# Optimization experiments

Hardware: AMD Instinct MI355X
Metric: run time of the kernel (lower is better)

The kernel has to match this reference:

```python
import jax, jax.numpy as jnp
import numpy as np

N = 100000          # active voxels
KS = 7              # kernel size per spatial dim
K = KS ** 3         # 343 kernel offsets
G = 64              # voxel grid extent
INPLANES = 128
PLANES = 128
D2 = PLANES // 4    # 32
EPS = 1e-5


def _build_neighbor_map(seed=0):
    # Random distinct voxel coordinates in a G^3 grid, then for every point and
    # every 7^3 offset find the index of the neighboring voxel (-1 if absent).
    rng = np.random.default_rng(seed)
    lin = rng.choice(G ** 3, size=N, replace=False)
    coords = np.stack(np.unravel_index(lin, (G, G, G)), axis=1).astype(np.int64)  # [N,3]
    keys = coords[:, 0] * G * G + coords[:, 1] * G + coords[:, 2]
    order = np.argsort(keys)
    skeys = keys[order]
    offs = np.arange(KS) - KS // 2
    off_grid = np.stack(np.meshgrid(offs, offs, offs, indexing='ij'), axis=-1).reshape(K, 3)
    q = coords[:, None, :] + off_grid[None, :, :]          # [N,K,3]
    inb = np.all((q >= 0) & (q < G), axis=-1)
    qk = q[..., 0] * G * G + q[..., 1] * G + q[..., 2]
    pos = np.searchsorted(skeys, qk)
    pos_c = np.clip(pos, 0, N - 1)
    found = inb & (skeys[pos_c] == qk)
    nbr = np.where(found, order[pos_c], -1).astype(np.int32)  # [N,K]
    return jnp.asarray(nbr)


def setup_inputs() -> dict:
    key = jax.random.key(0)
    k = jax.random.split(key, 4)
    feats = jax.random.normal(k[0], (N, INPLANES), jnp.float32)
    w1 = jax.random.normal(k[1], (INPLANES, D2), jnp.float32) / np.sqrt(INPLANES)
    w_conv = jax.random.normal(k[2], (K, D2, D2), jnp.float32) / np.sqrt(K * D2)
    w2 = jax.random.normal(k[3], (D2, PLANES), jnp.float32) / np.sqrt(D2)
    return {
        'feats': feats,
        'nbr': _build_neighbor_map(),
        'w1': w1,
        'ln1_g': jnp.ones((D2,), jnp.float32),
        'ln1_b': jnp.zeros((D2,), jnp.float32),
        'w_conv': w_conv,
        'w2': w2,
        'ln2_g': jnp.ones((PLANES,), jnp.float32),
        'ln2_b': jnp.zeros((PLANES,), jnp.float32),
    }


def _layernorm(x, g, b):
    m = jnp.mean(x, axis=-1, keepdims=True)
    v = jnp.var(x, axis=-1, keepdims=True)
    return (x - m) * jax.lax.rsqrt(v + EPS) * g + b


def _sparse_conv(x, nbr, w):
    # x: [N,d2], nbr: [N,K], w: [K,d2,d2]; gather-apply-scatter per kernel offset.
    def step(acc, inp):
        idx, wk = inp                                # idx: [N], wk: [d2,d2]
        valid = (idx >= 0).astype(x.dtype)[:, None]
        g = jnp.take(x, jnp.maximum(idx, 0), axis=0) * valid
        return acc + g @ wk, None
    acc0 = jnp.zeros((x.shape[0], w.shape[2]), x.dtype)
    out, _ = jax.lax.scan(step, acc0, (nbr.T, w))
    return out


def reference(feats, nbr, w1, ln1_g, ln1_b, w_conv, w2, ln2_g, ln2_b):
    shortcut = feats                                  # inplanes == planes -> Identity
    h = _layernorm(feats @ w1, ln1_g, ln1_b)          # unary_1: [N,d2]
    h = _sparse_conv(h, nbr, w_conv)                  # 7^3 sparse conv: [N,d2]
    h = _layernorm(h @ w2, ln2_g, ln2_b)              # unary_2: [N,planes]
    h = jax.nn.gelu(h, approximate=False)             # drop_path is Identity (rate 0)
    return h + shortcut
```

## Files before the change

kernel.cpp:

```cpp
#include <hip/hip_runtime.h>
#include <hip/hip_bf16.h>

#define N_PTS 100000
#define KOFF 343
#define EPS 1e-5f

typedef __hip_bfloat16 bf16;
typedef __attribute__((ext_vector_type(4))) float f32x4;
typedef __attribute__((ext_vector_type(16))) float f32x16;
typedef __attribute__((ext_vector_type(8))) short s16x8;

__global__ __launch_bounds__(256) void pack_kernel(const float* __restrict__ w_conv,
                                                   bf16* __restrict__ wpk) {
  int t = blockIdx.x * 256 + threadIdx.x;
  if (t >= KOFF * 128) return;
  int l = t & 63;
  int s = (t >> 6) & 1;
  int k = t >> 7;
  int col = l & 31;
  int kq = l >> 5;
  const float* wk = w_conv + k * 1024;
  s16x8 v;
  for (int j = 0; j < 8; ++j) {
    bf16 h = __float2bfloat16(wk[(s * 16 + kq * 8 + j) * 32 + col]);
    short sv;
    __builtin_memcpy(&sv, &h, 2);
    v[j] = sv;
  }
  *reinterpret_cast<s16x8*>(reinterpret_cast<char*>(wpk) + (size_t)t * 16) = v;
}

__global__ __launch_bounds__(256) void unary1_kernel(const float* __restrict__ feats,
    const float* __restrict__ w1, const float* __restrict__ g1,
    const float* __restrict__ b1, bf16* __restrict__ h1b) {
  __shared__ float sf[8][128];
  __shared__ float sw[128 * 32];
  int tid = threadIdx.x;
  int rbase = blockIdx.x * 8;
  for (int i = tid; i < 1024; i += 256)
    reinterpret_cast<f32x4*>(sw)[i] = reinterpret_cast<const f32x4*>(w1)[i];
  {
    int i = tid;
    int r = rbase + (i >> 5);
    f32x4 v = reinterpret_cast<const f32x4*>(feats)[(size_t)r * 32 + (i & 31)];
    reinterpret_cast<f32x4*>(&sf[0][0])[i] = v;
  }
  __syncthreads();
  int half = tid >> 5;
  int c = tid & 31;
  int r = rbase + half;
  const float* frow = sf[half];
  float acc = 0.f;
  #pragma unroll 8
  for (int kk = 0; kk < 128; ++kk)
    acc += frow[kk] * sw[kk * 32 + c];
  float s = acc, s2 = acc * acc;
  #pragma unroll
  for (int m = 16; m >= 1; m >>= 1) {
    s  += __shfl_xor(s,  m, 64);
    s2 += __shfl_xor(s2, m, 64);
  }
  float mean = s * (1.f / 32.f);
  float var  = s2 * (1.f / 32.f) - mean * mean;
  float y = (acc - mean) * rsqrtf(var + EPS) * g1[c] + b1[c];
  h1b[(size_t)r * 32 + c] = __float2bfloat16(y);
}

__global__ __launch_bounds__(256) void conv_kernel(const bf16* __restrict__ h1b,
    const int* __restrict__ nbr, const bf16* __restrict__ wpk,
    float* __restrict__ h2) {
  __shared__ int snbr[32 * 345];
  int tid = threadIdx.x;
  int wave = tid >> 6;
  int l = tid & 63;
  int col = l & 31;
  int kq = l >> 5;
  int pbase = blockIdx.x * 32;
  {
    const int* g = nbr + (size_t)pbase * KOFF;
    for (int i = tid; i < 32 * KOFF; i += 256) {
      unsigned row = (unsigned)i / KOFF;
      unsigned kk = (unsigned)i - row * KOFF;
      snbr[row * 345 + kk] = g[i];
    }
  }
  __syncthreads();
  int k0 = (KOFF * wave) >> 2;
  int k1 = (KOFF * (wave + 1)) >> 2;
  f32x16 acc;
  #pragma unroll
  for (int i = 0; i < 16; ++i) acc[i] = 0.f;
  const s16x8* wb = reinterpret_cast<const s16x8*>(wpk);
  const s16x8 zv = {0, 0, 0, 0, 0, 0, 0, 0};
  const int* myrow = snbr + col * 345;
  for (int kb = k0; kb < k1; kb += 4) {
    int id[4];
    s16x8 A0[4], A1[4], B0[4], B1[4];
    #pragma unroll
    for (int j = 0; j < 4; ++j) {
      int k = kb + j;
      id[j] = (k < k1) ? myrow[k] : -1;
    }
    #pragma unroll
    for (int j = 0; j < 4; ++j) {
      int k = kb + j;
      int kc = (k < k1) ? k : (k1 - 1);
      const s16x8* r = reinterpret_cast<const s16x8*>(h1b + (size_t)(id[j] < 0 ? 0 : id[j]) * 32);
      A0[j] = r[kq];
      A1[j] = r[2 + kq];
      B0[j] = wb[(size_t)kc * 128 + l];
      B1[j] = wb[(size_t)kc * 128 + 64 + l];
    }
    #pragma unroll
    for (int j = 0; j < 4; ++j) {
      s16x8 a0 = id[j] < 0 ? zv : A0[j];
      s16x8 a1 = id[j] < 0 ? zv : A1[j];
      acc = __builtin_amdgcn_mfma_f32_32x32x16_bf16(a0, B0[j], acc, 0, 0, 0);
      acc = __builtin_amdgcn_mfma_f32_32x32x16_bf16(a1, B1[j], acc, 0, 0, 0);
    }
  }
  __syncthreads();
  float* red = reinterpret_cast<float*>(snbr);
  #pragma unroll
  for (int reg = 0; reg < 16; ++reg) {
    int rrow = (reg & 3) + 8 * (reg >> 2) + 4 * kq;
    red[wave * 1024 + rrow * 32 + col] = acc[reg];
  }
  __syncthreads();
  const f32x4* rv = reinterpret_cast<const f32x4*>(red);
  f32x4 s = rv[tid] + rv[256 + tid] + rv[512 + tid] + rv[768 + tid];
  reinterpret_cast<f32x4*>(h2 + (size_t)pbase * 32)[tid] = s;
}

__global__ __launch_bounds__(256) void unary2_kernel(const float* __restrict__ h2,
    const float* __restrict__ w2, const float* __restrict__ g2,
    const float* __restrict__ b2, const float* __restrict__ feats,
    float* __restrict__ out) {
  int tid = threadIdx.x;
  int wave = tid >> 6;
  int l = tid & 63;
  int r = blockIdx.x * 4 + wave;
  const float* hrow = h2 + (size_t)r * 32;
  float acc0 = 0.f, acc1 = 0.f;
  #pragma unroll
  for (int q = 0; q < 8; ++q) {
    f32x4 hv = reinterpret_cast<const f32x4*>(hrow)[q];
    #pragma unroll
    for (int j = 0; j < 4; ++j) {
      int kk = q * 4 + j;
      float h = hv[j];
      acc0 += h * w2[kk * 128 + l];
      acc1 += h * w2[kk * 128 + 64 + l];
    }
  }
  float s = acc0 + acc1, s2 = acc0 * acc0 + acc1 * acc1;
  #pragma unroll
  for (int m = 32; m >= 1; m >>= 1) {
    s  += __shfl_xor(s,  m, 64);
    s2 += __shfl_xor(s2, m, 64);
  }
  float mean = s * (1.f / 128.f);
  float var  = s2 * (1.f / 128.f) - mean * mean;
  float inv = rsqrtf(var + EPS);
  float y0 = (acc0 - mean) * inv * g2[l] + b2[l];
  float y1 = (acc1 - mean) * inv * g2[64 + l] + b2[64 + l];
  float ge0 = 0.5f * y0 * (1.f + erff(y0 * 0.70710678118f));
  float ge1 = 0.5f * y1 * (1.f + erff(y1 * 0.70710678118f));
  out[(size_t)r * 128 + l]      = ge0 + feats[(size_t)r * 128 + l];
  out[(size_t)r * 128 + 64 + l] = ge1 + feats[(size_t)r * 128 + 64 + l];
}

extern "C" void kernel_launch(void* const* d_in, const int* in_sizes, int n_in,
                              void* d_out, int out_size, void* d_ws, size_t ws_size,
                              hipStream_t stream) {
  const float* feats  = (const float*)d_in[0];
  const int*   nbr    = (const int*)d_in[1];
  const float* w1     = (const float*)d_in[2];
  const float* ln1_g  = (const float*)d_in[3];
  const float* ln1_b  = (const float*)d_in[4];
  const float* w_conv = (const float*)d_in[5];
  const float* w2     = (const float*)d_in[6];
  const float* ln2_g  = (const float*)d_in[7];
  const float* ln2_b  = (const float*)d_in[8];
  float* out = (float*)d_out;
  char* ws = (char*)d_ws;
  bf16*  h1b = (bf16*)ws;
  bf16*  wpk = (bf16*)(ws + 6400000);
  float* h2  = (float*)(ws + 7102464);

  hipLaunchKernelGGL(pack_kernel,   dim3((KOFF * 128 + 255) / 256), dim3(256), 0, stream, w_conv, wpk);
  hipLaunchKernelGGL(unary1_kernel, dim3(N_PTS / 8),                dim3(256), 0, stream, feats, w1, ln1_g, ln1_b, h1b);
  hipLaunchKernelGGL(conv_kernel,   dim3(N_PTS / 32),               dim3(256), 0, stream, h1b, nbr, wpk, h2);
  hipLaunchKernelGGL(unary2_kernel, dim3(N_PTS / 4),                dim3(256), 0, stream, h2, w2, ln2_g, ln2_b, feats, out);
}
```

Baseline: 328.5 us.

## Transpose neighbor map and give each wave a full 32-point tile

Adds a kernel that transposes the [N,K] neighbor map into [K,N] so each wave can read neighbor indices for 32 points per offset with coalesced loads. The new conv kernel assigns one 32-point tile per wave over all 343 offsets, prefetching the next group of indices. This removes the LDS staging, the cross-wave reduction and the block barriers. The cost is an extra pass that reads and writes the full 137 MB index array, and the path runs only when the workspace is large enough.

Result: slower. 473.5 us (+44.1%).

```diff
diff --git a/kernel.cpp b/kernel.cpp
--- a/kernel.cpp
+++ b/kernel.cpp
@@ -4,6 +4,7 @@
 #define N_PTS 100000
 #define KOFF 343
 #define EPS 1e-5f
+#define NTILES 3125
 
 typedef __hip_bfloat16 bf16;
 typedef __attribute__((ext_vector_type(4))) float f32x4;
@@ -64,6 +65,86 @@
   float var  = s2 * (1.f / 32.f) - mean * mean;
   float y = (acc - mean) * rsqrtf(var + EPS) * g1[c] + b1[c];
   h1b[(size_t)r * 32 + c] = __float2bfloat16(y);
+}
+
+__global__ __launch_bounds__(256) void transpose_kernel(const int* __restrict__ nbr,
+                                                        int* __restrict__ nbrT) {
+  __shared__ int t[32][33];
+  int tx = threadIdx.x & 31;
+  int ty0 = threadIdx.x >> 5;
+  int n0 = blockIdx.x * 32;
+  int k0 = blockIdx.y * 32;
+  #pragma unroll
+  for (int q = 0; q < 4; ++q) {
+    int ty = ty0 + 8 * q;
+    int k = k0 + tx;
+    if (k < KOFF) t[ty][tx] = nbr[(size_t)(n0 + ty) * KOFF + k];
+  }
+  __syncthreads();
+  #pragma unroll
+  for (int q = 0; q < 4; ++q) {
+    int ky = ty0 + 8 * q;
+    if (k0 + ky < KOFF)
+      nbrT[(size_t)(k0 + ky) * N_PTS + n0 + tx] = t[tx][ky];
+  }
+}
+
+__global__ __launch_bounds__(256) void conv_t_kernel(const bf16* __restrict__ h1b,
+    const int* __restrict__ nbrT, const bf16* __restrict__ wpk,
+    float* __restrict__ h2) {
+  int tid = threadIdx.x;
+  int wave = tid >> 6;
+  int l = tid & 63;
+  int col = l & 31;
+  int kq = l >> 5;
+  int tile = blockIdx.x * 4 + wave;
+  if (tile >= NTILES) return;
+  int pbase = tile * 32;
+  const int* nbase = nbrT + pbase + col;
+  f32x16 acc;
+  #pragma unroll
+  for (int i = 0; i < 16; ++i) acc[i] = 0.f;
+  const s16x8* wb = reinterpret_cast<const s16x8*>(wpk);
+  const s16x8 zv = {0, 0, 0, 0, 0, 0, 0, 0};
+  int idc[4];
+  #pragma unroll
+  for (int j = 0; j < 4; ++j) idc[j] = nbase[(size_t)j * N_PTS];
+  for (int kb = 0; kb < KOFF; kb += 4) {
+    int idn[4];
+    #pragma unroll
+    for (int j = 0; j < 4; ++j) {
+      int kn = kb + 4 + j;
+      idn[j] = (kn < KOFF) ? nbase[(size_t)kn * N_PTS] : -1;
+    }
+    s16x8 A0[4], A1[4], B0[4], B1[4];
+    #pragma unroll
+    for (int j = 0; j < 4; ++j) {
+      int k = kb + j;
+      int kc = (k < KOFF) ? k : (KOFF - 1);
+      int id = (k < KOFF) ? idc[j] : -1;
+      const s16x8* r = reinterpret_cast<const s16x8*>(h1b + (size_t)(id < 0 ? 0 : id) * 32);
+      A0[j] = r[kq];
+      A1[j] = r[2 + kq];
+      B0[j] = wb[(size_t)kc * 128 + l];
+      B1[j] = wb[(size_t)kc * 128 + 64 + l];
+    }
+    #pragma unroll
+    for (int j = 0; j < 4; ++j) {
+      int k = kb + j;
+      int id = (k < KOFF) ? idc[j] : -1;
+      s16x8 a0 = id < 0 ? zv : A0[j];
+      s16x8 a1 = id < 0 ? zv : A1[j];
+      acc = __builtin_amdgcn_mfma_f32_32x32x16_bf16(a0, B0[j], acc, 0, 0, 0);
+      acc = __builtin_amdgcn_mfma_f32_32x32x16_bf16(a1, B1[j], acc, 0, 0, 0);
+    }
+    #pragma unroll
+    for (int j = 0; j < 4; ++j) idc[j] = idn[j];
+  }
+  #pragma unroll
+  for (int reg = 0; reg < 16; ++reg) {
+    int rrow = (reg & 3) + 8 * (reg >> 2) + 4 * kq;
+    h2[(size_t)(pbase + rrow) * 32 + col] = acc[reg];
+  }
 }
 
 __global__ __launch_bounds__(256) void conv_kernel(const bf16* __restrict__ h1b,
@@ -187,9 +268,16 @@
   bf16*  h1b = (bf16*)ws;
   bf16*  wpk = (bf16*)(ws + 6400000);
   float* h2  = (float*)(ws + 7102464);
+  int*   nbrT = (int*)(ws + 19902464);
+  const size_t need = 19902464ULL + 137200000ULL;
 
   hipLaunchKernelGGL(pack_kernel,   dim3((KOFF * 128 + 255) / 256), dim3(256), 0, stream, w_conv, wpk);
   hipLaunchKernelGGL(unary1_kernel, dim3(N_PTS / 8),                dim3(256), 0, stream, feats, w1, ln1_g, ln1_b, h1b);
-  hipLaunchKernelGGL(conv_kernel,   dim3(N_PTS / 32),               dim3(256), 0, stream, h1b, nbr, wpk, h2);
-  hipLaunchKernelGGL(unary2_kernel, dim3(N_PTS / 4),                dim3(256), 0, stream, h2, w2, ln2_g, ln2_b, feats, out);
-}
+  if (ws_size >= need) {
+    hipLaunchKernelGGL(transpose_kernel, dim3(NTILES, (KOFF + 31) / 32), dim3(256), 0, stream, nbr, nbrT);
+    hipLaunchKernelGGL(conv_t_kernel,    dim3((NTILES + 3) / 4),         dim3(256), 0, stream, h1b, nbrT, wpk, h2);
+  } else {
+    hipLaunchKernelGGL(conv_kernel,      dim3(NTILES),                   dim3(256), 0, stream, h1b, nbr, wpk, h2);
+  }
+  hipLaunchKernelGGL(unary2_kernel, dim3(N_PTS / 4), dim3(256), 0, stream, h2, w2, ln2_g, ln2_b, feats, out);
+}
```

## Transpose neighbor map and restructure conv to stream k-major indices

Applied to the files above, without the earlier changes.

Adds a kernel that transposes the [N,343] neighbor map into k-major layout in workspace. A new conv kernel uses it: each wave reads coalesced neighbor indices directly from global memory with a software prefetch two steps ahead, instead of staging the whole map in shared memory. Each block now covers two 32-point tiles, and each tile's offsets are split across two waves. This adds a full extra read and write of about 137 MB for the transpose, and falls back to the old kernel if the workspace is too small.

Result: slower. 455.8 us (+38.8%).

```diff
diff --git a/kernel.cpp b/kernel.cpp
--- a/kernel.cpp
+++ b/kernel.cpp
@@ -4,6 +4,7 @@
 #define N_PTS 100000
 #define KOFF 343
 #define EPS 1e-5f
+#define NTILES 3125
 
 typedef __hip_bfloat16 bf16;
 typedef __attribute__((ext_vector_type(4))) float f32x4;
@@ -64,6 +65,90 @@
   float var  = s2 * (1.f / 32.f) - mean * mean;
   float y = (acc - mean) * rsqrtf(var + EPS) * g1[c] + b1[c];
   h1b[(size_t)r * 32 + c] = __float2bfloat16(y);
+}
+
+__global__ __launch_bounds__(256) void transpose_kernel(const int* __restrict__ nbr,
+                                                        int* __restrict__ nbrT) {
+  __shared__ int t[32][129];
+  int n0 = blockIdx.x * 128;
+  int k0 = blockIdx.y * 32;
+  int tx = threadIdx.x & 31;
+  int ty = threadIdx.x >> 5;
+  int kmax = KOFF - k0;
+  #pragma unroll
+  for (int q = 0; q < 16; ++q) {
+    int r = ty + 8 * q;
+    int n = n0 + r;
+    if (n < N_PTS && tx < kmax) t[tx][r] = nbr[(size_t)n * KOFF + k0 + tx];
+  }
+  __syncthreads();
+  int wx = threadIdx.x & 127;
+  int wy = threadIdx.x >> 7;
+  #pragma unroll
+  for (int q = 0; q < 16; ++q) {
+    int kk = wy + 2 * q;
+    int n = n0 + wx;
+    if (kk < kmax && n < N_PTS) nbrT[(size_t)(k0 + kk) * N_PTS + n] = t[kk][wx];
+  }
+}
+
+__global__ __launch_bounds__(256, 6) void conv_t2_kernel(const bf16* __restrict__ h1b,
+    const int* __restrict__ nbrT, const bf16* __restrict__ wpk,
+    float* __restrict__ h2) {
+  __shared__ float red[4 * 1024];
+  int tid = threadIdx.x;
+  int wave = tid >> 6;
+  int l = tid & 63;
+  int col = l & 31;
+  int kq = l >> 5;
+  int tile = wave & 1;
+  int half = wave >> 1;
+  int pbase = blockIdx.x * 64 + tile * 32;
+  bool live = pbase < N_PTS;
+  const int* nbase = nbrT + pbase + col;
+  int k0 = (KOFF * half) >> 1;
+  int k1 = (KOFF * (half + 1)) >> 1;
+  f32x16 acc;
+  #pragma unroll
+  for (int i = 0; i < 16; ++i) acc[i] = 0.f;
+  const s16x8* wb = reinterpret_cast<const s16x8*>(wpk);
+  const s16x8 zv = {0, 0, 0, 0, 0, 0, 0, 0};
+  int id0 = live ? nbase[(size_t)k0 * N_PTS] : -1;
+  int id1 = (live && k0 + 1 < k1) ? nbase[(size_t)(k0 + 1) * N_PTS] : -1;
+  int id2 = (live && k0 + 2 < k1) ? nbase[(size_t)(k0 + 2) * N_PTS] : -1;
+  int id3 = (live && k0 + 3 < k1) ? nbase[(size_t)(k0 + 3) * N_PTS] : -1;
+  for (int kb = k0; kb < k1; kb += 2) {
+    int kc1 = (kb + 1 < k1) ? kb + 1 : kb;
+    const s16x8* r0 = reinterpret_cast<const s16x8*>(h1b + (size_t)(id0 < 0 ? 0 : id0) * 32);
+    const s16x8* r1 = reinterpret_cast<const s16x8*>(h1b + (size_t)(id1 < 0 ? 0 : id1) * 32);
+    s16x8 A00 = r0[kq], A01 = r0[2 + kq];
+    s16x8 A10 = r1[kq], A11 = r1[2 + kq];
+    s16x8 B00 = wb[(size_t)kb * 128 + l];
+    s16x8 B01 = wb[(size_t)kb * 128 + 64 + l];
+    s16x8 B10 = wb[(size_t)kc1 * 128 + l];
+    s16x8 B11 = wb[(size_t)kc1 * 128 + 64 + l];
+    int id4 = (live && kb + 4 < k1) ? nbase[(size_t)(kb + 4) * N_PTS] : -1;
+    int id5 = (live && kb + 5 < k1) ? nbase[(size_t)(kb + 5) * N_PTS] : -1;
+    s16x8 a;
+    a = id0 < 0 ? zv : A00; acc = __builtin_amdgcn_mfma_f32_32x32x16_bf16(a, B00, acc, 0, 0, 0);
+    a = id0 < 0 ? zv : A01; acc = __builtin_amdgcn_mfma_f32_32x32x16_bf16(a, B01, acc, 0, 0, 0);
+    a = id1 < 0 ? zv : A10; acc = __builtin_amdgcn_mfma_f32_32x32x16_bf16(a, B10, acc, 0, 0, 0);
+    a = id1 < 0 ? zv : A11; acc = __builtin_amdgcn_mfma_f32_32x32x16_bf16(a, B11, acc, 0, 0, 0);
+    id0 = id2; id1 = id3; id2 = id4; id3 = id5;
+  }
+  #pragma unroll
+  for (int reg = 0; reg < 16; ++reg) {
+    int rrow = (reg & 3) + 8 * (reg >> 2) + 4 * kq;
+    red[wave * 1024 + rrow * 32 + col] = acc[reg];
+  }
+  __syncthreads();
+  const f32x4* rv = reinterpret_cast<const f32x4*>(red);
+  f32x4 sA = rv[tid] + rv[512 + tid];
+  f32x4 sB = rv[256 + tid] + rv[768 + tid];
+  f32x4* o = reinterpret_cast<f32x4*>(h2 + (size_t)blockIdx.x * 2048);
+  int p0 = blockIdx.x * 64;
+  if (p0 + 32 <= N_PTS) o[tid] = sA;
+  if (p0 + 64 <= N_PTS) o[256 + tid] = sB;
 }
 
 __global__ __launch_bounds__(256) void conv_kernel(const bf16* __restrict__ h1b,
@@ -187,9 +272,16 @@
   bf16*  h1b = (bf16*)ws;
   bf16*  wpk = (bf16*)(ws + 6400000);
   float* h2  = (float*)(ws + 7102464);
+  int*   nbrT = (int*)(ws + 19902464);
+  const size_t need = 19902464ULL + 137200000ULL;
 
   hipLaunchKernelGGL(pack_kernel,   dim3((KOFF * 128 + 255) / 256), dim3(256), 0, stream, w_conv, wpk);
   hipLaunchKernelGGL(unary1_kernel, dim3(N_PTS / 8),                dim3(256), 0, stream, feats, w1, ln1_g, ln1_b, h1b);
-  hipLaunchKernelGGL(conv_kernel,   dim3(N_PTS / 32),               dim3(256), 0, stream, h1b, nbr, wpk, h2);
-  hipLaunchKernelGGL(unary2_kernel, dim3(N_PTS / 4),                dim3(256), 0, stream, h2, w2, ln2_g, ln2_b, feats, out);
-}
+  if (ws_size >= need) {
+    hipLaunchKernelGGL(transpose_kernel, dim3((N_PTS + 127) / 128, (KOFF + 31) / 32), dim3(256), 0, stream, nbr, nbrT);
+    hipLaunchKernelGGL(conv_t2_kernel,   dim3((NTILES + 1) / 2),                      dim3(256), 0, stream, h1b, nbrT, wpk, h2);
+  } else {
+    hipLaunchKernelGGL(conv_kernel,      dim3(NTILES),                                dim3(256), 0, stream, h1b, nbr, wpk, h2);
+  }
+  hipLaunchKernelGGL(unary2_kernel, dim3(N_PTS / 4), dim3(256), 0, stream, h2, w2, ln2_g, ln2_b, feats, out);
+}
```

## Stage neighbor indices in four rounds with zero-row sentinel to shrink LDS

Applied to the files above, without the earlier changes.

The conv kernel now stages the neighbor map in four chunks of about 86 offsets into a 16KB shared buffer, down from the full 44KB one, which allows higher occupancy (launch bounds request 4 blocks). Missing neighbors are remapped to a zero row appended after h1b, so the per-element select on invalid gathers goes away. Index loads for the next group are prefetched before the MFMAs. The cost is extra barriers between rounds and less overlap of index staging with compute.

Result: slower. 386.1 us (+17.5%).

```diff
diff --git a/kernel.cpp b/kernel.cpp
--- a/kernel.cpp
+++ b/kernel.cpp
@@ -4,6 +4,8 @@
 #define N_PTS 100000
 #define KOFF 343
 #define EPS 1e-5f
+#define NTILES 3125
+#define SSTRIDE 87
 
 typedef __hip_bfloat16 bf16;
 typedef __attribute__((ext_vector_type(4))) float f32x4;
@@ -37,6 +39,8 @@
   __shared__ float sw[128 * 32];
   int tid = threadIdx.x;
   int rbase = blockIdx.x * 8;
+  if (blockIdx.x == 0 && tid < 16)
+    reinterpret_cast<int*>(h1b)[N_PTS * 16 + tid] = 0;
   for (int i = tid; i < 1024; i += 256)
     reinterpret_cast<f32x4*>(sw)[i] = reinterpret_cast<const f32x4*>(w1)[i];
   {
@@ -66,61 +70,92 @@
   h1b[(size_t)r * 32 + c] = __float2bfloat16(y);
 }
 
-__global__ __launch_bounds__(256) void conv_kernel(const bf16* __restrict__ h1b,
+template<int KCNT, int KBASE>
+__device__ __forceinline__ void stage_round(const int* __restrict__ g,
+                                            int* __restrict__ snbr, int wave, int l) {
+  #pragma unroll
+  for (int rr = 0; rr < 8; ++rr) {
+    int row = wave * 8 + rr;
+    const int* src = g + row * KOFF + KBASE;
+    if (l < KCNT) {
+      int v = src[l];
+      snbr[row * SSTRIDE + l] = v < 0 ? N_PTS : v;
+    }
+    if (64 + l < KCNT) {
+      int v = src[64 + l];
+      snbr[row * SSTRIDE + 64 + l] = v < 0 ? N_PTS : v;
+    }
+  }
+}
+
+template<int KCNT, int KBASE>
+__device__ __forceinline__ void process_round(const int* __restrict__ snbr,
+    const bf16* __restrict__ h1b, const s16x8* __restrict__ wb,
+    f32x16& acc, int wave, int l, int col, int kq) {
+  int k0 = (KCNT * wave) >> 2;
+  int k1 = (KCNT * (wave + 1)) >> 2;
+  const int* myrow = snbr + col * SSTRIDE;
+  int id[4];
+  #pragma unroll
+  for (int j = 0; j < 4; ++j) id[j] = (k0 + j < k1) ? myrow[k0 + j] : N_PTS;
+  for (int kb = k0; kb < k1; kb += 4) {
+    s16x8 A0[4], A1[4], B0[4], B1[4];
+    #pragma unroll
+    for (int j = 0; j < 4; ++j) {
+      const s16x8* r = reinterpret_cast<const s16x8*>(h1b + (size_t)id[j] * 32);
+      A0[j] = r[kq];
+      A1[j] = r[2 + kq];
+      int kc = (kb + j < k1) ? kb + j : k1 - 1;
+      B0[j] = wb[(size_t)(KBASE + kc) * 128 + l];
+      B1[j] = wb[(size_t)(KBASE + kc) * 128 + 64 + l];
+    }
+    int idn[4];
+    #pragma unroll
+    for (int j = 0; j < 4; ++j) idn[j] = (kb + 4 + j < k1) ? myrow[kb + 4 + j] : N_PTS;
+    #pragma unroll
+    for (int j = 0; j < 4; ++j) {
+      acc = __builtin_amdgcn_mfma_f32_32x32x16_bf16(A0[j], B0[j], acc, 0, 0, 0);
+      acc = __builtin_amdgcn_mfma_f32_32x32x16_bf16(A1[j], B1[j], acc, 0, 0, 0);
+    }
+    #pragma unroll
+    for (int j = 0; j < 4; ++j) id[j] = idn[j];
+  }
+}
+
+__global__ __launch_bounds__(256, 4) void conv_s2_kernel(const bf16* __restrict__ h1b,
     const int* __restrict__ nbr, const bf16* __restrict__ wpk,
     float* __restrict__ h2) {
-  __shared__ int snbr[32 * 345];
+  __shared__ int sbuf[4096];
   int tid = threadIdx.x;
   int wave = tid >> 6;
   int l = tid & 63;
   int col = l & 31;
   int kq = l >> 5;
   int pbase = blockIdx.x * 32;
-  {
-    const int* g = nbr + (size_t)pbase * KOFF;
-    for (int i = tid; i < 32 * KOFF; i += 256) {
-      unsigned row = (unsigned)i / KOFF;
-      unsigned kk = (unsigned)i - row * KOFF;
-      snbr[row * 345 + kk] = g[i];
-    }
-  }
-  __syncthreads();
-  int k0 = (KOFF * wave) >> 2;
-  int k1 = (KOFF * (wave + 1)) >> 2;
+  const int* g = nbr + (size_t)pbase * KOFF;
+  const s16x8* wb = reinterpret_cast<const s16x8*>(wpk);
   f32x16 acc;
   #pragma unroll
   for (int i = 0; i < 16; ++i) acc[i] = 0.f;
-  const s16x8* wb = reinterpret_cast<const s16x8*>(wpk);
-  const s16x8 zv = {0, 0, 0, 0, 0, 0, 0, 0};
-  const int* myrow = snbr + col * 345;
-  for (int kb = k0; kb < k1; kb += 4) {
-    int id[4];
-    s16x8 A0[4], A1[4], B0[4], B1[4];
-    #pragma unroll
-    for (int j = 0; j < 4; ++j) {
-      int k = kb + j;
-      id[j] = (k < k1) ? myrow[k] : -1;
-    }
-    #pragma unroll
-    for (int j = 0; j < 4; ++j) {
-      int k = kb + j;
-      int kc = (k < k1) ? k : (k1 - 1);
-      const s16x8* r = reinterpret_cast<const s16x8*>(h1b + (size_t)(id[j] < 0 ? 0 : id[j]) * 32);
-      A0[j] = r[kq];
-      A1[j] = r[2 + kq];
-      B0[j] = wb[(size_t)kc * 128 + l];
-      B1[j] = wb[(size_t)kc * 128 + 64 + l];
-    }
-    #pragma unroll
-    for (int j = 0; j < 4; ++j) {
-      s16x8 a0 = id[j] < 0 ? zv : A0[j];
-      s16x8 a1 = id[j] < 0 ? zv : A1[j];
-      acc = __builtin_amdgcn_mfma_f32_32x32x16_bf16(a0, B0[j], acc, 0, 0, 0);
-      acc = __builtin_amdgcn_mfma_f32_32x32x16_bf16(a1, B1[j], acc, 0, 0, 0);
-    }
-  }
-  __syncthreads();
-  float* red = reinterpret_cast<float*>(snbr);
+
+  stage_round<86, 0>(g, sbuf, wave, l);
+  __syncthreads();
+  process_round<86, 0>(sbuf, h1b, wb, acc, wave, l, col, kq);
+  __syncthreads();
+  stage_round<86, 86>(g, sbuf, wave, l);
+  __syncthreads();
+  process_round<86, 86>(sbuf, h1b, wb, acc, wave, l, col, kq);
+  __syncthreads();
+  stage_round<86, 172>(g, sbuf, wave, l);
+  __syncthreads();
+  process_round<86, 172>(sbuf, h1b, wb, acc, wave, l, col, kq);
+  __syncthreads();
+  stage_round<85, 258>(g, sbuf, wave, l);
+  __syncthreads();
+  process_round<85, 258>(sbuf, h1b, wb, acc, wave, l, col, kq);
+  __syncthreads();
+
+  float* red = reinterpret_cast<float*>(sbuf);
   #pragma unroll
   for (int reg = 0; reg < 16; ++reg) {
     int rrow = (reg & 3) + 8 * (reg >> 2) + 4 * kq;
@@ -185,11 +220,11 @@
   float* out = (float*)d_out;
   char* ws = (char*)d_ws;
   bf16*  h1b = (bf16*)ws;
-  bf16*  wpk = (bf16*)(ws + 6400000);
-  float* h2  = (float*)(ws + 7102464);
-
-  hipLaunchKernelGGL(pack_kernel,   dim3((KOFF * 128 + 255) / 256), dim3(256), 0, stream, w_conv, wpk);
-  hipLaunchKernelGGL(unary1_kernel, dim3(N_PTS / 8),                dim3(256), 0, stream, feats, w1, ln1_g, ln1_b, h1b);
-  hipLaunchKernelGGL(conv_kernel,   dim3(N_PTS / 32),               dim3(256), 0, stream, h1b, nbr, wpk, h2);
-  hipLaunchKernelGGL(unary2_kernel, dim3(N_PTS / 4),                dim3(256), 0, stream, h2, w2, ln2_g, ln2_b, feats, out);
-}
+  bf16*  wpk = (bf16*)(ws + 6400064);
+  float* h2  = (float*)(ws + 7102528);
+
+  hipLaunchKernelGGL(pack_kernel,    dim3((KOFF * 128 + 255) / 256), dim3(256), 0, stream, w_conv, wpk);
+  hipLaunchKernelGGL(unary1_kernel,  dim3(N_PTS / 8),                dim3(256), 0, stream, feats, w1, ln1_g, ln1_b, h1b);
+  hipLaunchKernelGGL(conv_s2_kernel, dim3(NTILES),                   dim3(256), 0, stream, h1b, nbr, wpk, h2);
+  hipLaunchKernelGGL(unary2_kernel,  dim3(N_PTS / 4),                dim3(256), 0, stream, h2, w2, ln2_g, ln2_b, feats, out);
+}
```
